# Optimization experiments

Measured on AMD Instinct MI355X. Metric: run time of the kernel, lower is better.

The kernel has to match this reference:

```python
import jax, jax.numpy as jnp
import numpy as np

ALP = 0.1
LAM = 1.0
N_NODES = 100000
N_EDGES = 800000
D_FEAT = 64


def setup_inputs() -> dict:
    key = jax.random.key(0)
    ks = jax.random.split(key, 7)
    h = jax.random.normal(ks[0], (N_NODES, D_FEAT), dtype=jnp.float32)
    ini_h = jax.random.normal(ks[1], (N_NODES, D_FEAT), dtype=jnp.float32)
    bef_A = jax.random.uniform(ks[2], (N_NODES, 1), dtype=jnp.float32)
    aft_A = jax.random.uniform(ks[3], (N_NODES, 1), dtype=jnp.float32)
    bef_X = jax.random.uniform(ks[4], (N_NODES, 1), dtype=jnp.float32)
    src = jax.random.randint(ks[5], (N_EDGES,), 0, N_NODES, dtype=jnp.int32)
    dst = jax.random.randint(ks[6], (N_EDGES,), 0, N_NODES, dtype=jnp.int32)
    return {"h": h, "ini_h": ini_h, "bef_A": bef_A, "aft_A": aft_A,
            "bef_X": bef_X, "src": src, "dst": dst}


def reference(h, ini_h, bef_A, aft_A, bef_X, src, dst):
    # propagation_lt:
    #   ini_h' = ini_h * bef_X
    #   agg    = A @ (h * aft_A)   (copy_u/sum over edges src->dst)
    #   out    = alp*lam * (agg * bef_A) + (1-alp)*h + alp*ini_h'
    pre_h = h
    msg = (h * aft_A)[src]                                  # [E, D]
    agg = jax.ops.segment_sum(msg, dst, num_segments=N_NODES)  # [N, D]
    agg = agg * bef_A
    return ALP * LAM * agg + (1.0 - ALP) * pre_h + ALP * (ini_h * bef_X)
```

## Files before the change

### kernel.cpp

```cpp
#include <hip/hip_runtime.h>

#define ALP 0.1f
#define OMA 0.9f
#define D 64
#define DV 16
#define SH 9
#define NODES_PER_B 512
#define CAP 16
#define OVF_MAX 65536

__device__ __forceinline__ unsigned short f2b(float f) {
    unsigned u = __float_as_uint(f);
    unsigned r = u + 0x7fffu + ((u >> 16) & 1u);
    return (unsigned short)(r >> 16);
}
__device__ __forceinline__ float b2f(unsigned short u) {
    return __uint_as_float(((unsigned)u) << 16);
}

__global__ void vsgc_msg(const float4* __restrict__ h4, const float* __restrict__ aft_A,
                         ushort4* __restrict__ msgb, int* __restrict__ zeroRegion,
                         int zeroWords, int n16) {
    if (blockIdx.x == 0) {
        for (int j = threadIdx.x; j < zeroWords; j += blockDim.x) zeroRegion[j] = 0;
    }
    int i = blockIdx.x * blockDim.x + threadIdx.x;
    if (i >= n16) return;
    float w = aft_A[i >> 4];
    float4 v = h4[i];
    msgb[i] = make_ushort4(f2b(v.x * w), f2b(v.y * w), f2b(v.z * w), f2b(v.w * w));
}

__global__ __launch_bounds__(256) void p1_scatter(const int4* __restrict__ src4,
                                                  const int4* __restrict__ dst4,
                                                  int* __restrict__ gcnt,
                                                  int* __restrict__ buckets,
                                                  int2* __restrict__ ovf,
                                                  int* __restrict__ ovfCnt,
                                                  int E, int NB, int BCAP) {
    __shared__ int cnt[256], gbase[256], pos[256];
    int tid = threadIdx.x;
    cnt[tid] = 0; pos[tid] = 0;
    __syncthreads();
    int nInt4 = (E + 3) >> 2;
    int i0 = blockIdx.x * 512 + tid;
    int i1 = i0 + 256;
    bool v0 = i0 < nInt4, v1 = i1 < nInt4;
    int4 s0 = make_int4(0,0,0,0), d0 = s0, s1 = s0, d1 = s0;
    if (v0) { s0 = src4[i0]; d0 = dst4[i0]; }
    if (v1) { s1 = src4[i1]; d1 = dst4[i1]; }
    int e0 = i0 << 2, e1 = i1 << 2;
    int ss[8] = {s0.x, s0.y, s0.z, s0.w, s1.x, s1.y, s1.z, s1.w};
    int dd[8] = {d0.x, d0.y, d0.z, d0.w, d1.x, d1.y, d1.z, d1.w};
    bool ok[8];
#pragma unroll
    for (int k = 0; k < 4; ++k) { ok[k] = v0 && (e0 + k < E); ok[4 + k] = v1 && (e1 + k < E); }
#pragma unroll
    for (int k = 0; k < 8; ++k) if (ok[k]) atomicAdd(&cnt[dd[k] >> SH], 1);
    __syncthreads();
    if (tid < NB && cnt[tid] > 0) gbase[tid] = atomicAdd(&gcnt[tid], cnt[tid]);
    __syncthreads();
    int pp[8];
#pragma unroll
    for (int k = 0; k < 8; ++k)
        pp[k] = ok[k] ? (gbase[dd[k] >> SH] + atomicAdd(&pos[dd[k] >> SH], 1)) : 0;
#pragma unroll
    for (int k = 0; k < 8; ++k) {
        if (!ok[k]) continue;
        int b = dd[k] >> SH;
        int pkt = (ss[k] << SH) | (dd[k] & (NODES_PER_B - 1));
        if (pp[k] < BCAP) buckets[(size_t)b * BCAP + pp[k]] = pkt;
        else { int o = atomicAdd(ovfCnt, 1); if (o < OVF_MAX) ovf[o] = make_int2(ss[k], dd[k]); }
    }
}

__global__ __launch_bounds__(512) void p2_ell(const int* __restrict__ buckets,
                                              const int* __restrict__ gcnt,
                                              int* __restrict__ ell,
                                              int* __restrict__ cnt_g,
                                              int2* __restrict__ ovf,
                                              int* __restrict__ ovfCnt,
                                              int N, int BCAP) {
    __shared__ int npos[NODES_PER_B];
    int b = blockIdx.x, tid = threadIdx.x;
    npos[tid] = 0;
    __syncthreads();
    int nb = min(gcnt[b], BCAP);
    const int4* bp4 = (const int4*)(buckets + (size_t)b * BCAP);
    int nIter = (nb + 3) >> 2;
    for (int i4 = tid; i4 < nIter; i4 += 512) {
        int4 r4 = bp4[i4];
        int base = i4 << 2;
        int pk[4] = {r4.x, r4.y, r4.z, r4.w};
#pragma unroll
        for (int k = 0; k < 4; ++k) {
            if (base + k >= nb) break;
            int pkt = pk[k];
            int l = pkt & (NODES_PER_B - 1);
            int s = (int)(((unsigned)pkt) >> SH);
            int slot = atomicAdd(&npos[l], 1);
            int node = (b << SH) + l;
            if (slot < CAP) ell[(size_t)node * CAP + slot] = s;
            else { int o = atomicAdd(ovfCnt, 1); if (o < OVF_MAX) ovf[o] = make_int2(s, node); }
        }
    }
    __syncthreads();
    int node = (b << SH) + tid;
    if (node < N) cnt_g[node] = npos[tid];
}

__global__ __launch_bounds__(256) void vsgc_gather_ell(const ushort4* __restrict__ msgb,
                                                       const float4* __restrict__ h4,
                                                       const float4* __restrict__ ini4,
                                                       const float* __restrict__ bef_A,
                                                       const float* __restrict__ bef_X,
                                                       const int* __restrict__ cnt_g,
                                                       const int* __restrict__ ell,
                                                       float4* __restrict__ out4, int N) {
    int g = (blockIdx.x * blockDim.x + threadIdx.x) >> 6;
    if (g >= N) return;
    int lane = threadIdx.x & 63;
    int w = lane >> 4;
    int q = lane & 15;
    size_t ridx = (size_t)g * DV + q;
    int ev = ell[(size_t)g * CAP + q];
    int n = min(cnt_g[g], CAP);
    float4 hv = h4[ridx];
    float4 iv = ini4[ridx];
    float cb = ALP * bef_A[g];
    float bx = ALP * bef_X[g];
    float4 acc = make_float4(0.f, 0.f, 0.f, 0.f);
#pragma unroll
    for (int k = 0; k < 4; ++k) {
        int idx = w + 4 * k;
        int s = __shfl(ev, idx);
        unsigned su = min((unsigned)s, (unsigned)(N - 1));
        float m = (idx < n) ? 1.f : 0.f;
        ushort4 mm = msgb[(size_t)su * DV + q];
        acc.x += m * b2f(mm.x);
        acc.y += m * b2f(mm.y);
        acc.z += m * b2f(mm.z);
        acc.w += m * b2f(mm.w);
    }
    acc.x += __shfl_xor(acc.x, 16); acc.y += __shfl_xor(acc.y, 16);
    acc.z += __shfl_xor(acc.z, 16); acc.w += __shfl_xor(acc.w, 16);
    acc.x += __shfl_xor(acc.x, 32); acc.y += __shfl_xor(acc.y, 32);
    acc.z += __shfl_xor(acc.z, 32); acc.w += __shfl_xor(acc.w, 32);
    if (w == 0) {
        float4 o;
        o.x = OMA * hv.x + bx * iv.x + cb * acc.x;
        o.y = OMA * hv.y + bx * iv.y + cb * acc.y;
        o.z = OMA * hv.z + bx * iv.z + cb * acc.z;
        o.w = OMA * hv.w + bx * iv.w + cb * acc.w;
        out4[ridx] = o;
    }
}

__global__ void vsgc_ovf(const float4* __restrict__ h4,
                         const float* __restrict__ aft_A,
                         const float* __restrict__ bef_A,
                         const int2* __restrict__ ovf,
                         const int* __restrict__ ovfCnt,
                         float* __restrict__ out) {
    int total = min(*ovfCnt, OVF_MAX);
    int stride = blockDim.x * gridDim.x;
    for (int t = blockIdx.x * blockDim.x + threadIdx.x; t < total * 16; t += stride) {
        int e = t >> 4, q = t & 15;
        int2 r = ovf[e];
        float c = ALP * aft_A[r.x] * bef_A[r.y];
        float4 hv = h4[(size_t)r.x * DV + q];
        float* op = out + (size_t)r.y * D + (q << 2);
        unsafeAtomicAdd(op + 0, c * hv.x);
        unsafeAtomicAdd(op + 1, c * hv.y);
        unsafeAtomicAdd(op + 2, c * hv.z);
        unsafeAtomicAdd(op + 3, c * hv.w);
    }
}

__global__ void vsgc_init(const float4* __restrict__ h, const float4* __restrict__ ini_h,
                          const float* __restrict__ bef_X, float4* __restrict__ out, int n4) {
    int i = blockIdx.x * blockDim.x + threadIdx.x;
    if (i >= n4) return;
    int node = i >> 4;
    float bx = ALP * bef_X[node];
    float4 hv = h[i];
    float4 iv = ini_h[i];
    float4 o;
    o.x = OMA * hv.x + bx * iv.x;
    o.y = OMA * hv.y + bx * iv.y;
    o.z = OMA * hv.z + bx * iv.z;
    o.w = OMA * hv.w + bx * iv.w;
    out[i] = o;
}
__global__ void vsgc_edges_atomic(const float4* __restrict__ h,
                                  const float* __restrict__ aft_A,
                                  const float* __restrict__ bef_A,
                                  const int* __restrict__ src,
                                  const int* __restrict__ dst,
                                  float* __restrict__ out, int E) {
    int tid = blockIdx.x * blockDim.x + threadIdx.x;
    int e = tid >> 4;
    int q = tid & 15;
    if (e >= E) return;
    int s = src[e];
    int d = dst[e];
    float c = ALP * aft_A[s] * bef_A[d];
    float4 hv = h[(size_t)s * DV + q];
    float* op = out + (size_t)d * D + (q << 2);
    unsafeAtomicAdd(op + 0, c * hv.x);
    unsafeAtomicAdd(op + 1, c * hv.y);
    unsafeAtomicAdd(op + 2, c * hv.z);
    unsafeAtomicAdd(op + 3, c * hv.w);
}

extern "C" void kernel_launch(void* const* d_in, const int* in_sizes, int n_in,
                              void* d_out, int out_size, void* d_ws, size_t ws_size,
                              hipStream_t stream) {
    const float* h     = (const float*)d_in[0];
    const float* ini_h = (const float*)d_in[1];
    const float* bef_A = (const float*)d_in[2];
    const float* aft_A = (const float*)d_in[3];
    const float* bef_X = (const float*)d_in[4];
    const int*   src   = (const int*)d_in[5];
    const int*   dst   = (const int*)d_in[6];
    float* out = (float*)d_out;

    const int N = in_sizes[0] / D;
    const int E = in_sizes[5];
    const int t = 256;

    int NB = (N + NODES_PER_B - 1) >> SH;
    int perB = (NB > 0) ? E / NB : 0;
    int BCAP = ((perB + perB / 4 + 256) + 3) & ~3;

    size_t o_gcnt = 0;
    size_t o_ovfc = 256 * 4;
    size_t o_ovf  = ((o_ovfc + 64 * 4 + 255) / 256) * 256;
    size_t o_cnt  = o_ovf + (size_t)OVF_MAX * 8;
    size_t o_ell  = ((o_cnt + (size_t)N * 4 + 255) / 256) * 256;
    size_t o_bkt  = ((o_ell + (size_t)N * CAP * 4 + 255) / 256) * 256;
    size_t o_msg  = ((o_bkt + (size_t)NB * BCAP * 4 + 255) / 256) * 256;
    size_t need   = o_msg + (size_t)N * 128;

    if (NB <= 256 && N <= (1 << (31 - SH)) && ws_size >= need) {
        int*  gcnt  = (int*)((char*)d_ws + o_gcnt);
        int*  ovfC  = (int*)((char*)d_ws + o_ovfc);
        int2* ovf   = (int2*)((char*)d_ws + o_ovf);
        int*  cnt_g = (int*)((char*)d_ws + o_cnt);
        int*  ell   = (int*)((char*)d_ws + o_ell);
        int*  bkt   = (int*)((char*)d_ws + o_bkt);
        ushort4* msgb = (ushort4*)((char*)d_ws + o_msg);

        int zeroWords = (int)(o_ovf / 4);
        int n16 = N * DV;
        vsgc_msg<<<(n16 + t - 1) / t, t, 0, stream>>>(
            (const float4*)h, aft_A, msgb, (int*)d_ws, zeroWords, n16);

        int nInt4 = (E + 3) >> 2;
        int p1blocks = (nInt4 + 511) / 512;
        p1_scatter<<<p1blocks, 256, 0, stream>>>(
            (const int4*)src, (const int4*)dst, gcnt, bkt, ovf, ovfC, E, NB, BCAP);

        p2_ell<<<NB, 512, 0, stream>>>(bkt, gcnt, ell, cnt_g, ovf, ovfC, N, BCAP);

        long long threadsTotal = (long long)N * 64;
        vsgc_gather_ell<<<(int)((threadsTotal + t - 1) / t), t, 0, stream>>>(
            msgb, (const float4*)h, (const float4*)ini_h, bef_A, bef_X,
            cnt_g, ell, (float4*)out, N);

        vsgc_ovf<<<32, t, 0, stream>>>((const float4*)h, aft_A, bef_A, ovf, ovfC, out);
    } else {
        int n4 = N * DV;
        vsgc_init<<<(n4 + t - 1) / t, t, 0, stream>>>(
            (const float4*)h, (const float4*)ini_h, bef_X, (float4*)out, n4);
        long long total = (long long)E * DV;
        vsgc_edges_atomic<<<(int)((total + t - 1) / t), t, 0, stream>>>(
            (const float4*)h, aft_A, bef_A, src, dst, out, E);
    }
}
```

Measured before the change: 162.5 us.

## Fuse ELL build and gather into per-bucket shared-memory atomic accumulation

Replaces the two-stage path (bucket-to-ELL construction, then a per-node ELL gather) with a single kernel per 256-node bucket. Each bucket's edge packets are read directly and the bf16 messages are accumulated into a 64KB shared-memory tile with LDS float atomics, using a rotated column layout to avoid bank conflicts. The epilogue then applies the combine and writes the output. This drops the ELL arrays, one kernel launch and the per-node cap overflow path. In exchange it relies heavily on shared-memory atomics, and with 391 blocks of 1024 threads it may leave occupancy low.

```diff
diff --git a/kernel.cpp b/kernel.cpp
--- a/kernel.cpp
+++ b/kernel.cpp
@@ -4,9 +4,8 @@
 #define OMA 0.9f
 #define D 64
 #define DV 16
-#define SH 9
-#define NODES_PER_B 512
-#define CAP 16
+#define SH 8
+#define BNODES 256
 #define OVF_MAX 65536
 
 __device__ __forceinline__ unsigned short f2b(float f) {
@@ -38,9 +37,10 @@
                                                   int2* __restrict__ ovf,
                                                   int* __restrict__ ovfCnt,
                                                   int E, int NB, int BCAP) {
-    __shared__ int cnt[256], gbase[256], pos[256];
+    __shared__ int cnt[512], gbase[512], pos[512];
     int tid = threadIdx.x;
-    cnt[tid] = 0; pos[tid] = 0;
+    cnt[tid] = 0; cnt[tid + 256] = 0;
+    pos[tid] = 0; pos[tid + 256] = 0;
     __syncthreads();
     int nInt4 = (E + 3) >> 2;
     int i0 = blockIdx.x * 512 + tid;
@@ -58,7 +58,8 @@
 #pragma unroll
     for (int k = 0; k < 8; ++k) if (ok[k]) atomicAdd(&cnt[dd[k] >> SH], 1);
     __syncthreads();
-    if (tid < NB && cnt[tid] > 0) gbase[tid] = atomicAdd(&gcnt[tid], cnt[tid]);
+    for (int b = tid; b < NB; b += 256)
+        if (cnt[b] > 0) gbase[b] = atomicAdd(&gcnt[b], cnt[b]);
     __syncthreads();
     int pp[8];
 #pragma unroll
@@ -68,90 +69,73 @@
     for (int k = 0; k < 8; ++k) {
         if (!ok[k]) continue;
         int b = dd[k] >> SH;
-        int pkt = (ss[k] << SH) | (dd[k] & (NODES_PER_B - 1));
+        int pkt = (ss[k] << SH) | (dd[k] & (BNODES - 1));
         if (pp[k] < BCAP) buckets[(size_t)b * BCAP + pp[k]] = pkt;
         else { int o = atomicAdd(ovfCnt, 1); if (o < OVF_MAX) ovf[o] = make_int2(ss[k], dd[k]); }
     }
 }
 
-__global__ __launch_bounds__(512) void p2_ell(const int* __restrict__ buckets,
-                                              const int* __restrict__ gcnt,
-                                              int* __restrict__ ell,
-                                              int* __restrict__ cnt_g,
-                                              int2* __restrict__ ovf,
-                                              int* __restrict__ ovfCnt,
-                                              int N, int BCAP) {
-    __shared__ int npos[NODES_PER_B];
+__global__ __launch_bounds__(1024) void p2_gather(const int* __restrict__ buckets,
+                                                  const int* __restrict__ gcnt,
+                                                  const ushort4* __restrict__ msgb,
+                                                  const float4* __restrict__ h4,
+                                                  const float4* __restrict__ ini4,
+                                                  const float* __restrict__ bef_A,
+                                                  const float* __restrict__ bef_X,
+                                                  float4* __restrict__ out4,
+                                                  int N, int BCAP) {
+    __shared__ float acc[BNODES * 64];
     int b = blockIdx.x, tid = threadIdx.x;
-    npos[tid] = 0;
+    for (int k = tid; k < BNODES * 64; k += 1024) acc[k] = 0.f;
     __syncthreads();
     int nb = min(gcnt[b], BCAP);
-    const int4* bp4 = (const int4*)(buckets + (size_t)b * BCAP);
-    int nIter = (nb + 3) >> 2;
-    for (int i4 = tid; i4 < nIter; i4 += 512) {
-        int4 r4 = bp4[i4];
-        int base = i4 << 2;
-        int pk[4] = {r4.x, r4.y, r4.z, r4.w};
-#pragma unroll
-        for (int k = 0; k < 4; ++k) {
-            if (base + k >= nb) break;
-            int pkt = pk[k];
-            int l = pkt & (NODES_PER_B - 1);
-            int s = (int)(((unsigned)pkt) >> SH);
-            int slot = atomicAdd(&npos[l], 1);
-            int node = (b << SH) + l;
-            if (slot < CAP) ell[(size_t)node * CAP + slot] = s;
-            else { int o = atomicAdd(ovfCnt, 1); if (o < OVF_MAX) ovf[o] = make_int2(s, node); }
+    const int* bp = buckets + (size_t)b * BCAP;
+    int grp = tid >> 4;
+    int q = tid & 15;
+    for (int i = grp; i < nb; i += 128) {
+        int i2 = i + 64;
+        bool has2 = i2 < nb;
+        int pkt1 = bp[i];
+        int pkt2 = has2 ? bp[i2] : pkt1;
+        int l1 = pkt1 & (BNODES - 1);
+        int s1v = (int)(((unsigned)pkt1) >> SH);
+        int l2 = pkt2 & (BNODES - 1);
+        int s2v = (int)(((unsigned)pkt2) >> SH);
+        ushort4 m1 = msgb[(size_t)s1v * DV + q];
+        ushort4 m2 = msgb[(size_t)s2v * DV + q];
+        int base1 = l1 << 6;
+        atomicAdd(&acc[base1 + ((q + 0  + l1) & 63)], b2f(m1.x));
+        atomicAdd(&acc[base1 + ((q + 16 + l1) & 63)], b2f(m1.y));
+        atomicAdd(&acc[base1 + ((q + 32 + l1) & 63)], b2f(m1.z));
+        atomicAdd(&acc[base1 + ((q + 48 + l1) & 63)], b2f(m1.w));
+        if (has2) {
+            int base2 = l2 << 6;
+            atomicAdd(&acc[base2 + ((q + 0  + l2) & 63)], b2f(m2.x));
+            atomicAdd(&acc[base2 + ((q + 16 + l2) & 63)], b2f(m2.y));
+            atomicAdd(&acc[base2 + ((q + 32 + l2) & 63)], b2f(m2.z));
+            atomicAdd(&acc[base2 + ((q + 48 + l2) & 63)], b2f(m2.w));
         }
     }
     __syncthreads();
-    int node = (b << SH) + tid;
-    if (node < N) cnt_g[node] = npos[tid];
-}
-
-__global__ __launch_bounds__(256) void vsgc_gather_ell(const ushort4* __restrict__ msgb,
-                                                       const float4* __restrict__ h4,
-                                                       const float4* __restrict__ ini4,
-                                                       const float* __restrict__ bef_A,
-                                                       const float* __restrict__ bef_X,
-                                                       const int* __restrict__ cnt_g,
-                                                       const int* __restrict__ ell,
-                                                       float4* __restrict__ out4, int N) {
-    int g = (blockIdx.x * blockDim.x + threadIdx.x) >> 6;
-    if (g >= N) return;
-    int lane = threadIdx.x & 63;
-    int w = lane >> 4;
-    int q = lane & 15;
-    size_t ridx = (size_t)g * DV + q;
-    int ev = ell[(size_t)g * CAP + q];
-    int n = min(cnt_g[g], CAP);
-    float4 hv = h4[ridx];
-    float4 iv = ini4[ridx];
-    float cb = ALP * bef_A[g];
-    float bx = ALP * bef_X[g];
-    float4 acc = make_float4(0.f, 0.f, 0.f, 0.f);
-#pragma unroll
-    for (int k = 0; k < 4; ++k) {
-        int idx = w + 4 * k;
-        int s = __shfl(ev, idx);
-        unsigned su = min((unsigned)s, (unsigned)(N - 1));
-        float m = (idx < n) ? 1.f : 0.f;
-        ushort4 mm = msgb[(size_t)su * DV + q];
-        acc.x += m * b2f(mm.x);
-        acc.y += m * b2f(mm.y);
-        acc.z += m * b2f(mm.z);
-        acc.w += m * b2f(mm.w);
-    }
-    acc.x += __shfl_xor(acc.x, 16); acc.y += __shfl_xor(acc.y, 16);
-    acc.z += __shfl_xor(acc.z, 16); acc.w += __shfl_xor(acc.w, 16);
-    acc.x += __shfl_xor(acc.x, 32); acc.y += __shfl_xor(acc.y, 32);
-    acc.z += __shfl_xor(acc.z, 32); acc.w += __shfl_xor(acc.w, 32);
-    if (w == 0) {
+    for (int idx = tid; idx < BNODES * 16; idx += 1024) {
+        int l = idx >> 4, c = idx & 15;
+        int g = (b << SH) + l;
+        if (g >= N) break;
+        int base = l << 6;
+        float a0 = acc[base + ((c + 0  + l) & 63)];
+        float a1 = acc[base + ((c + 16 + l) & 63)];
+        float a2 = acc[base + ((c + 32 + l) & 63)];
+        float a3 = acc[base + ((c + 48 + l) & 63)];
+        float cb = ALP * bef_A[g];
+        float bx = ALP * bef_X[g];
+        size_t ridx = (size_t)g * DV + c;
+        float4 hv = h4[ridx];
+        float4 iv = ini4[ridx];
         float4 o;
-        o.x = OMA * hv.x + bx * iv.x + cb * acc.x;
-        o.y = OMA * hv.y + bx * iv.y + cb * acc.y;
-        o.z = OMA * hv.z + bx * iv.z + cb * acc.z;
-        o.w = OMA * hv.w + bx * iv.w + cb * acc.w;
+        o.x = OMA * hv.x + bx * iv.x + cb * a0;
+        o.y = OMA * hv.y + bx * iv.y + cb * a1;
+        o.z = OMA * hv.z + bx * iv.z + cb * a2;
+        o.w = OMA * hv.w + bx * iv.w + cb * a3;
         out4[ridx] = o;
     }
 }
@@ -229,25 +213,21 @@
     const int E = in_sizes[5];
     const int t = 256;
 
-    int NB = (N + NODES_PER_B - 1) >> SH;
+    int NB = (N + BNODES - 1) >> SH;
     int perB = (NB > 0) ? E / NB : 0;
     int BCAP = ((perB + perB / 4 + 256) + 3) & ~3;
 
     size_t o_gcnt = 0;
-    size_t o_ovfc = 256 * 4;
+    size_t o_ovfc = 512 * 4;
     size_t o_ovf  = ((o_ovfc + 64 * 4 + 255) / 256) * 256;
-    size_t o_cnt  = o_ovf + (size_t)OVF_MAX * 8;
-    size_t o_ell  = ((o_cnt + (size_t)N * 4 + 255) / 256) * 256;
-    size_t o_bkt  = ((o_ell + (size_t)N * CAP * 4 + 255) / 256) * 256;
+    size_t o_bkt  = o_ovf + (size_t)OVF_MAX * 8;
     size_t o_msg  = ((o_bkt + (size_t)NB * BCAP * 4 + 255) / 256) * 256;
     size_t need   = o_msg + (size_t)N * 128;
 
-    if (NB <= 256 && N <= (1 << (31 - SH)) && ws_size >= need) {
+    if (NB <= 512 && N <= (1 << 23) && ws_size >= need) {
         int*  gcnt  = (int*)((char*)d_ws + o_gcnt);
         int*  ovfC  = (int*)((char*)d_ws + o_ovfc);
         int2* ovf   = (int2*)((char*)d_ws + o_ovf);
-        int*  cnt_g = (int*)((char*)d_ws + o_cnt);
-        int*  ell   = (int*)((char*)d_ws + o_ell);
         int*  bkt   = (int*)((char*)d_ws + o_bkt);
         ushort4* msgb = (ushort4*)((char*)d_ws + o_msg);
 
@@ -261,12 +241,9 @@
         p1_scatter<<<p1blocks, 256, 0, stream>>>(
             (const int4*)src, (const int4*)dst, gcnt, bkt, ovf, ovfC, E, NB, BCAP);
 
-        p2_ell<<<NB, 512, 0, stream>>>(bkt, gcnt, ell, cnt_g, ovf, ovfC, N, BCAP);
-
-        long long threadsTotal = (long long)N * 64;
-        vsgc_gather_ell<<<(int)((threadsTotal + t - 1) / t), t, 0, stream>>>(
-            msgb, (const float4*)h, (const float4*)ini_h, bef_A, bef_X,
-            cnt_g, ell, (float4*)out, N);
+        p2_gather<<<NB, 1024, 0, stream>>>(
+            bkt, gcnt, msgb, (const float4*)h, (const float4*)ini_h,
+            bef_A, bef_X, (float4*)out, N, BCAP);
 
         vsgc_ovf<<<32, t, 0, stream>>>((const float4*)h, aft_A, bef_A, ovf, ovfC, out);
     } else {
```

Result: slower. 464.2 us (+185.6%).

## Fuse message and bucket-scatter kernels, process two nodes per wavefront in gather

Applied to the files above, without the earlier changes.

Merges the bf16 message-conversion kernel and the edge-bucket scatter into one launch, with blocks split by index, and moves the workspace zeroing to a hipMemsetAsync. The gather kernel now handles two destination nodes per 64-lane wavefront, interleaving their neighbor loads to raise memory-level parallelism and halve the wave count. This removes one kernel launch and the serial zeroing done by block 0, but adds a memset call and more registers per thread in the gather.

```diff
diff --git a/kernel.cpp b/kernel.cpp
--- a/kernel.cpp
+++ b/kernel.cpp
@@ -18,28 +18,24 @@
     return __uint_as_float(((unsigned)u) << 16);
 }
 
-__global__ void vsgc_msg(const float4* __restrict__ h4, const float* __restrict__ aft_A,
-                         ushort4* __restrict__ msgb, int* __restrict__ zeroRegion,
-                         int zeroWords, int n16) {
-    if (blockIdx.x == 0) {
-        for (int j = threadIdx.x; j < zeroWords; j += blockDim.x) zeroRegion[j] = 0;
-    }
-    int i = blockIdx.x * blockDim.x + threadIdx.x;
-    if (i >= n16) return;
-    float w = aft_A[i >> 4];
-    float4 v = h4[i];
-    msgb[i] = make_ushort4(f2b(v.x * w), f2b(v.y * w), f2b(v.z * w), f2b(v.w * w));
-}
-
-__global__ __launch_bounds__(256) void p1_scatter(const int4* __restrict__ src4,
-                                                  const int4* __restrict__ dst4,
-                                                  int* __restrict__ gcnt,
-                                                  int* __restrict__ buckets,
-                                                  int2* __restrict__ ovf,
-                                                  int* __restrict__ ovfCnt,
-                                                  int E, int NB, int BCAP) {
+__global__ __launch_bounds__(256) void vsgc_msgp1(
+        const float4* __restrict__ h4, const float* __restrict__ aft_A,
+        ushort4* __restrict__ msgb, int n16,
+        const int4* __restrict__ src4, const int4* __restrict__ dst4,
+        int* __restrict__ gcnt, int* __restrict__ buckets,
+        int2* __restrict__ ovf, int* __restrict__ ovfCnt,
+        int E, int NB, int BCAP, int p1Blocks) {
+    int tid = threadIdx.x;
+    if ((int)blockIdx.x >= p1Blocks) {
+        int i = (blockIdx.x - p1Blocks) * 256 + tid;
+        if (i < n16) {
+            float w = aft_A[i >> 4];
+            float4 v = h4[i];
+            msgb[i] = make_ushort4(f2b(v.x * w), f2b(v.y * w), f2b(v.z * w), f2b(v.w * w));
+        }
+        return;
+    }
     __shared__ int cnt[256], gbase[256], pos[256];
-    int tid = threadIdx.x;
     cnt[tid] = 0; pos[tid] = 0;
     __syncthreads();
     int nInt4 = (E + 3) >> 2;
@@ -117,42 +113,70 @@
                                                        const int* __restrict__ cnt_g,
                                                        const int* __restrict__ ell,
                                                        float4* __restrict__ out4, int N) {
-    int g = (blockIdx.x * blockDim.x + threadIdx.x) >> 6;
-    if (g >= N) return;
+    int wid = (blockIdx.x * blockDim.x + threadIdx.x) >> 6;
+    int g0 = wid * 2;
+    if (g0 >= N) return;
+    int g1 = g0 + 1;
+    bool has1 = g1 < N;
+    int g1c = has1 ? g1 : g0;
     int lane = threadIdx.x & 63;
     int w = lane >> 4;
     int q = lane & 15;
-    size_t ridx = (size_t)g * DV + q;
-    int ev = ell[(size_t)g * CAP + q];
-    int n = min(cnt_g[g], CAP);
-    float4 hv = h4[ridx];
-    float4 iv = ini4[ridx];
-    float cb = ALP * bef_A[g];
-    float bx = ALP * bef_X[g];
-    float4 acc = make_float4(0.f, 0.f, 0.f, 0.f);
+    size_t r0 = (size_t)g0 * DV + q;
+    size_t r1 = (size_t)g1c * DV + q;
+    int ev0 = ell[(size_t)g0 * CAP + q];
+    int ev1 = ell[(size_t)g1c * CAP + q];
+    int n0 = min(cnt_g[g0], CAP);
+    int n1 = has1 ? min(cnt_g[g1c], CAP) : 0;
+    float4 hv0 = h4[r0];
+    float4 hv1 = h4[r1];
+    float4 iv0 = ini4[r0];
+    float4 iv1 = ini4[r1];
+    float cb0 = ALP * bef_A[g0];
+    float bx0 = ALP * bef_X[g0];
+    float cb1 = ALP * bef_A[g1c];
+    float bx1 = ALP * bef_X[g1c];
+    float4 a0 = make_float4(0.f, 0.f, 0.f, 0.f);
+    float4 a1 = a0;
+    unsigned clampN = (unsigned)(N - 1);
 #pragma unroll
     for (int k = 0; k < 4; ++k) {
         int idx = w + 4 * k;
-        int s = __shfl(ev, idx);
-        unsigned su = min((unsigned)s, (unsigned)(N - 1));
-        float m = (idx < n) ? 1.f : 0.f;
-        ushort4 mm = msgb[(size_t)su * DV + q];
-        acc.x += m * b2f(mm.x);
-        acc.y += m * b2f(mm.y);
-        acc.z += m * b2f(mm.z);
-        acc.w += m * b2f(mm.w);
-    }
-    acc.x += __shfl_xor(acc.x, 16); acc.y += __shfl_xor(acc.y, 16);
-    acc.z += __shfl_xor(acc.z, 16); acc.w += __shfl_xor(acc.w, 16);
-    acc.x += __shfl_xor(acc.x, 32); acc.y += __shfl_xor(acc.y, 32);
-    acc.z += __shfl_xor(acc.z, 32); acc.w += __shfl_xor(acc.w, 32);
+        int s0 = __shfl(ev0, idx);
+        int s1 = __shfl(ev1, idx);
+        unsigned su0 = min((unsigned)s0, clampN);
+        unsigned su1 = min((unsigned)s1, clampN);
+        float m0 = (idx < n0) ? 1.f : 0.f;
+        float m1 = (idx < n1) ? 1.f : 0.f;
+        ushort4 q0 = msgb[(size_t)su0 * DV + q];
+        ushort4 q1 = msgb[(size_t)su1 * DV + q];
+        a0.x += m0 * b2f(q0.x); a0.y += m0 * b2f(q0.y);
+        a0.z += m0 * b2f(q0.z); a0.w += m0 * b2f(q0.w);
+        a1.x += m1 * b2f(q1.x); a1.y += m1 * b2f(q1.y);
+        a1.z += m1 * b2f(q1.z); a1.w += m1 * b2f(q1.w);
+    }
+    a0.x += __shfl_xor(a0.x, 16); a0.y += __shfl_xor(a0.y, 16);
+    a0.z += __shfl_xor(a0.z, 16); a0.w += __shfl_xor(a0.w, 16);
+    a0.x += __shfl_xor(a0.x, 32); a0.y += __shfl_xor(a0.y, 32);
+    a0.z += __shfl_xor(a0.z, 32); a0.w += __shfl_xor(a0.w, 32);
+    a1.x += __shfl_xor(a1.x, 16); a1.y += __shfl_xor(a1.y, 16);
+    a1.z += __shfl_xor(a1.z, 16); a1.w += __shfl_xor(a1.w, 16);
+    a1.x += __shfl_xor(a1.x, 32); a1.y += __shfl_xor(a1.y, 32);
+    a1.z += __shfl_xor(a1.z, 32); a1.w += __shfl_xor(a1.w, 32);
     if (w == 0) {
         float4 o;
-        o.x = OMA * hv.x + bx * iv.x + cb * acc.x;
-        o.y = OMA * hv.y + bx * iv.y + cb * acc.y;
-        o.z = OMA * hv.z + bx * iv.z + cb * acc.z;
-        o.w = OMA * hv.w + bx * iv.w + cb * acc.w;
-        out4[ridx] = o;
+        o.x = OMA * hv0.x + bx0 * iv0.x + cb0 * a0.x;
+        o.y = OMA * hv0.y + bx0 * iv0.y + cb0 * a0.y;
+        o.z = OMA * hv0.z + bx0 * iv0.z + cb0 * a0.z;
+        o.w = OMA * hv0.w + bx0 * iv0.w + cb0 * a0.w;
+        out4[r0] = o;
+    } else if (w == 1 && has1) {
+        float4 o;
+        o.x = OMA * hv1.x + bx1 * iv1.x + cb1 * a1.x;
+        o.y = OMA * hv1.y + bx1 * iv1.y + cb1 * a1.y;
+        o.z = OMA * hv1.z + bx1 * iv1.z + cb1 * a1.z;
+        o.w = OMA * hv1.w + bx1 * iv1.w + cb1 * a1.w;
+        out4[r1] = o;
     }
 }
 
@@ -251,19 +275,21 @@
         int*  bkt   = (int*)((char*)d_ws + o_bkt);
         ushort4* msgb = (ushort4*)((char*)d_ws + o_msg);
 
-        int zeroWords = (int)(o_ovf / 4);
+        hipMemsetAsync(d_ws, 0, o_ovf, stream);
+
         int n16 = N * DV;
-        vsgc_msg<<<(n16 + t - 1) / t, t, 0, stream>>>(
-            (const float4*)h, aft_A, msgb, (int*)d_ws, zeroWords, n16);
-
         int nInt4 = (E + 3) >> 2;
-        int p1blocks = (nInt4 + 511) / 512;
-        p1_scatter<<<p1blocks, 256, 0, stream>>>(
-            (const int4*)src, (const int4*)dst, gcnt, bkt, ovf, ovfC, E, NB, BCAP);
+        int p1Blocks = (nInt4 + 511) / 512;
+        int msgBlocks = (n16 + t - 1) / t;
+        vsgc_msgp1<<<p1Blocks + msgBlocks, t, 0, stream>>>(
+            (const float4*)h, aft_A, msgb, n16,
+            (const int4*)src, (const int4*)dst, gcnt, bkt, ovf, ovfC,
+            E, NB, BCAP, p1Blocks);
 
         p2_ell<<<NB, 512, 0, stream>>>(bkt, gcnt, ell, cnt_g, ovf, ovfC, N, BCAP);
 
-        long long threadsTotal = (long long)N * 64;
+        long long waves = (N + 1) / 2;
+        long long threadsTotal = waves * 64;
         vsgc_gather_ell<<<(int)((threadsTotal + t - 1) / t), t, 0, stream>>>(
             msgb, (const float4*)h, (const float4*)ini_h, bef_A, bef_X,
             cnt_g, ell, (float4*)out, N);
```

New measurement: 162.3 us. About the same (-0.1%).
